# Performance work log

Hardware: AMD Instinct MI355X
Metric: run time of the kernel (lower is better)

The kernel has to match this reference:

```python
import jax, jax.numpy as jnp
import numpy as np

B, S, H, L, NH, F, V = 8, 512, 768, 12, 12, 3072, 21128
DH = H // NH
SEP = 102
NEG = -1e9  # eager BERT additive mask: (1-mask)*large_negative


def _ln(x, g, b, eps=1e-12):
    m = jnp.mean(x, axis=-1, keepdims=True)
    v = jnp.var(x, axis=-1, keepdims=True)
    return (x - m) * jax.lax.rsqrt(v + eps) * g + b


def _mask_bias(input_ids):
    # prefix-LM mask: tokens <= first SEP fully bidirectional; suffix causal + sees prefix
    hit = input_ids == SEP                      # [B,S]
    has_sep = jnp.any(hit, axis=1)              # [B]
    first = jnp.argmax(hit, axis=1)             # [B] (first SEP position)
    sep = jnp.minimum(first, S - 2)             # clamp as in torch code
    pos = jnp.arange(S)
    i = pos[None, :, None]
    j = pos[None, None, :]
    sb = sep[:, None, None]
    vis = (j <= sb) | ((i > sb) & (j <= i))     # [B,S,S]
    vis = jnp.where(has_sep[:, None, None], vis, True)  # no SEP -> full ones
    return jnp.where(vis, 0.0, NEG).astype(jnp.float32)[:, None]  # [B,1,S,S]


def setup_inputs():
    key = jax.random.key(0)
    ks = jax.random.split(key, 4)
    input_ids = jax.random.randint(ks[0], (B, S), 0, V)
    sep_pos = jax.random.randint(ks[1], (B,), 32, 128)
    input_ids = input_ids.at[jnp.arange(B), sep_pos].set(SEP)
    labels = jax.random.randint(ks[2], (B, S), 0, V)
    pk = jax.random.split(ks[3], 10)
    n = lambda k, sh: jax.random.normal(k, sh, jnp.float32) * 0.02
    return dict(
        input_ids=input_ids, labels=labels,
        word_emb=n(pk[0], (V, H)), pos_emb=n(pk[1], (S, H)), type_emb=n(pk[2], (2, H)),
        emb_g=jnp.ones((H,), jnp.float32), emb_b=jnp.zeros((H,), jnp.float32),
        Wq=n(pk[3], (L, H, H)), bq=jnp.zeros((L, H), jnp.float32),
        Wk=n(pk[4], (L, H, H)), bk=jnp.zeros((L, H), jnp.float32),
        Wv=n(pk[5], (L, H, H)), bv=jnp.zeros((L, H), jnp.float32),
        Wo=n(pk[6], (L, H, H)), bo=jnp.zeros((L, H), jnp.float32),
        ln1_g=jnp.ones((L, H), jnp.float32), ln1_b=jnp.zeros((L, H), jnp.float32),
        W1=n(pk[7], (L, H, F)), b1=jnp.zeros((L, F), jnp.float32),
        W2=n(pk[8], (L, F, H)), b2=jnp.zeros((L, H), jnp.float32),
        ln2_g=jnp.ones((L, H), jnp.float32), ln2_b=jnp.zeros((L, H), jnp.float32),
        cls_W=n(pk[9], (H, V)), cls_b=jnp.zeros((V,), jnp.float32),
    )


def reference(input_ids, labels, word_emb, pos_emb, type_emb, emb_g, emb_b,
              Wq, bq, Wk, bk, Wv, bv, Wo, bo, ln1_g, ln1_b,
              W1, b1, W2, b2, ln2_g, ln2_b, cls_W, cls_b):
    bias = _mask_bias(input_ids)                               # [B,1,S,S]
    x = word_emb[input_ids] + pos_emb[None, :S] + type_emb[0]  # [B,S,H]
    x = _ln(x, emb_g, emb_b)

    def layer(h, p):
        wq, bq_, wk, bk_, wv, bv_, wo, bo_, g1, g1b, w1, bb1, w2, bb2, g2, g2b = p
        heads = lambda t: t.reshape(B, S, NH, DH).transpose(0, 2, 1, 3)
        q = heads(h @ wq + bq_)
        k = heads(h @ wk + bk_)
        v = heads(h @ wv + bv_)
        scores = jnp.einsum('bhqd,bhkd->bhqk', q, k) / np.sqrt(DH).astype(np.float32) + bias
        probs = jax.nn.softmax(scores, axis=-1)
        ctx = jnp.einsum('bhqk,bhkd->bhqd', probs, v).transpose(0, 2, 1, 3).reshape(B, S, H)
        h = _ln(h + ctx @ wo + bo_, g1, g1b)
        ffn = jax.nn.gelu(h @ w1 + bb1, approximate=False) @ w2 + bb2
        h = _ln(h + ffn, g2, g2b)
        return h, None

    x, _ = jax.lax.scan(layer, x, (Wq, bq, Wk, bk, Wv, bv, Wo, bo,
                                   ln1_g, ln1_b, W1, b1, W2, b2, ln2_g, ln2_b))
    logits = x @ cls_W + cls_b                                 # [B,S,V]

    # per-sample CE: mean over tokens after first SEP; full-sequence CE if no SEP
    logp = jax.nn.log_softmax(logits, axis=-1)
    ce = -jnp.take_along_axis(logp, labels[..., None], axis=-1)[..., 0]  # [B,S]
    hit = input_ids == SEP
    has_sep = jnp.any(hit, axis=1)
    first = jnp.argmax(hit, axis=1)
    pos = jnp.arange(S)[None]
    m = jnp.where(has_sep[:, None], pos > first[:, None], True).astype(ce.dtype)
    per_sample = jnp.sum(ce * m, axis=1) / jnp.sum(m, axis=1)
    return jnp.mean(per_sample)
```

## Files before the change

### kernel.cpp

```cpp
#include <hip/hip_runtime.h>
#include <math.h>

typedef unsigned short ushort;
typedef __bf16 bf16x8 __attribute__((ext_vector_type(8)));
typedef float f32x4 __attribute__((ext_vector_type(4)));

constexpr int Bb  = 8;
constexpr int Ss  = 512;
constexpr int Hh  = 768;
constexpr int Ll  = 12;
constexpr int NHh = 12;
constexpr int Ff  = 3072;
constexpr int Vv  = 21128;
constexpr int DHh = 64;
constexpr int Mm  = Bb * Ss;
constexpr int SEP_ID = 102;
constexpr int VP  = 21504;
constexpr int NCH = 24;
constexpr int TPC = 7;
constexpr int QKVN = 3 * Hh;
constexpr float LSE_SHIFT = 20.0f;

static __device__ __forceinline__ ushort f2bf(float f) {
    unsigned u = __float_as_uint(f);
    unsigned r = (u + 0x7fffu + ((u >> 16) & 1u)) >> 16;
    return (ushort)r;
}
static __device__ __forceinline__ float bf2f(unsigned x) {
    return __uint_as_float(x << 16);
}

__global__ __launch_bounds__(512) void sep_kernel(const int* __restrict__ ids,
                                                  int* __restrict__ info)
{
    int b = blockIdx.x;
    int t = threadIdx.x;
    int v = (ids[b * Ss + t] == SEP_ID) ? t : 0x7FFFFFFF;
    #pragma unroll
    for (int off = 32; off; off >>= 1) {
        int o = __shfl_xor(v, off);
        v = min(v, o);
    }
    __shared__ int wmin[8];
    int lane = t & 63, wid = t >> 6;
    if (lane == 0) wmin[wid] = v;
    __syncthreads();
    if (t == 0) {
        int first = wmin[0];
        #pragma unroll
        for (int w = 1; w < 8; w++) first = min(first, wmin[w]);
        int has = (first != 0x7FFFFFFF) ? 1 : 0;
        info[b * 4 + 0] = first;
        info[b * 4 + 1] = has;
        info[b * 4 + 2] = has ? min(first, Ss - 2) : (Ss + 1);
    }
}

__global__ __launch_bounds__(256) void embed_ln_kernel(
    const int* __restrict__ ids, const float* __restrict__ we,
    const float* __restrict__ pe, const float* __restrict__ te,
    const float* __restrict__ g, const float* __restrict__ bp,
    float* __restrict__ x, ushort* __restrict__ xb)
{
    int tok = blockIdx.x;
    int s = tok & (Ss - 1);
    int tid = threadIdx.x;
    int id = ids[tok];
    float e[3];
    #pragma unroll
    for (int r = 0; r < 3; r++) {
        int h = tid + (r << 8);
        e[r] = we[(size_t)id * Hh + h] + pe[(size_t)s * Hh + h] + te[h];
    }
    float sum = e[0] + e[1] + e[2];
    float sq  = fmaf(e[0], e[0], fmaf(e[1], e[1], e[2] * e[2]));
    #pragma unroll
    for (int off = 32; off; off >>= 1) {
        sum += __shfl_xor(sum, off);
        sq  += __shfl_xor(sq, off);
    }
    __shared__ float red[8];
    int lane = tid & 63, wid = tid >> 6;
    if (lane == 0) { red[wid] = sum; red[4 + wid] = sq; }
    __syncthreads();
    sum = red[0] + red[1] + red[2] + red[3];
    sq  = red[4] + red[5] + red[6] + red[7];
    float mean = sum * (1.0f / Hh);
    float var  = sq * (1.0f / Hh) - mean * mean;
    float rstd = rsqrtf(var + 1e-12f);
    #pragma unroll
    for (int r = 0; r < 3; r++) {
        int h = tid + (r << 8);
        float v = (e[r] - mean) * rstd * g[h] + bp[h];
        x[(size_t)tok * Hh + h] = v;
        xb[(size_t)tok * Hh + h] = f2bf(v);
    }
}

__global__ __launch_bounds__(256) void resid_ln_kernel(
    const float* __restrict__ resid, const float* __restrict__ y,
    const float* __restrict__ g, const float* __restrict__ bp,
    float* __restrict__ out, ushort* __restrict__ outb)
{
    int tok = blockIdx.x;
    int tid = threadIdx.x;
    float e[3];
    #pragma unroll
    for (int r = 0; r < 3; r++) {
        int h = tid + (r << 8);
        size_t idx = (size_t)tok * Hh + h;
        e[r] = resid[idx] + y[idx];
    }
    float sum = e[0] + e[1] + e[2];
    float sq  = fmaf(e[0], e[0], fmaf(e[1], e[1], e[2] * e[2]));
    #pragma unroll
    for (int off = 32; off; off >>= 1) {
        sum += __shfl_xor(sum, off);
        sq  += __shfl_xor(sq, off);
    }
    __shared__ float red[8];
    int lane = tid & 63, wid = tid >> 6;
    if (lane == 0) { red[wid] = sum; red[4 + wid] = sq; }
    __syncthreads();
    sum = red[0] + red[1] + red[2] + red[3];
    sq  = red[4] + red[5] + red[6] + red[7];
    float mean = sum * (1.0f / Hh);
    float var  = sq * (1.0f / Hh) - mean * mean;
    float rstd = rsqrtf(var + 1e-12f);
    #pragma unroll
    for (int r = 0; r < 3; r++) {
        int h = tid + (r << 8);
        float v = (e[r] - mean) * rstd * g[h] + bp[h];
        out[(size_t)tok * Hh + h] = v;
        outb[(size_t)tok * Hh + h] = f2bf(v);
    }
}

__global__ __launch_bounds__(256) void resid_ln4_kernel(
    const float* __restrict__ resid, const float* __restrict__ p,
    const float* __restrict__ bias, const float* __restrict__ g,
    const float* __restrict__ bp,
    float* __restrict__ out, ushort* __restrict__ outb)
{
    const size_t MHl = (size_t)Mm * Hh;
    int tok = blockIdx.x;
    int tid = threadIdx.x;
    float e[3];
    #pragma unroll
    for (int r = 0; r < 3; r++) {
        int h = tid + (r << 8);
        size_t idx = (size_t)tok * Hh + h;
        float acc = resid[idx] + bias[h];
        acc += p[idx];
        acc += p[MHl + idx];
        acc += p[2 * MHl + idx];
        acc += p[3 * MHl + idx];
        e[r] = acc;
    }
    float sum = e[0] + e[1] + e[2];
    float sq  = fmaf(e[0], e[0], fmaf(e[1], e[1], e[2] * e[2]));
    #pragma unroll
    for (int off = 32; off; off >>= 1) {
        sum += __shfl_xor(sum, off);
        sq  += __shfl_xor(sq, off);
    }
    __shared__ float red[8];
    int lane = tid & 63, wid = tid >> 6;
    if (lane == 0) { red[wid] = sum; red[4 + wid] = sq; }
    __syncthreads();
    sum = red[0] + red[1] + red[2] + red[3];
    sq  = red[4] + red[5] + red[6] + red[7];
    float mean = sum * (1.0f / Hh);
    float var  = sq * (1.0f / Hh) - mean * mean;
    float rstd = rsqrtf(var + 1e-12f);
    #pragma unroll
    for (int r = 0; r < 3; r++) {
        int h = tid + (r << 8);
        float v = (e[r] - mean) * rstd * g[h] + bp[h];
        out[(size_t)tok * Hh + h] = v;
        outb[(size_t)tok * Hh + h] = f2bf(v);
    }
}

__global__ __launch_bounds__(256) void transpose_kernel(
    const float* __restrict__ W, ushort* __restrict__ Wt, int K, int N)
{
    __shared__ float ts[32][33];
    int n0 = blockIdx.x * 32, k0 = blockIdx.y * 32;
    int tx = threadIdx.x & 31, ty = threadIdx.x >> 5;
    #pragma unroll
    for (int i = 0; i < 32; i += 8)
        ts[ty + i][tx] = W[(size_t)(k0 + ty + i) * N + n0 + tx];
    __syncthreads();
    #pragma unroll
    for (int i = 0; i < 32; i += 8)
        Wt[(size_t)(n0 + ty + i) * K + k0 + tx] = f2bf(ts[tx][ty + i]);
}

__global__ __launch_bounds__(256) void transpose4_kernel(
    const float* __restrict__ s0, const float* __restrict__ s1,
    const float* __restrict__ s2, const float* __restrict__ s3,
    ushort* __restrict__ dst)
{
    const float* srcs[4] = { s0, s1, s2, s3 };
    const float* W = srcs[blockIdx.z];
    ushort* Wt = dst + (size_t)blockIdx.z * Hh * Hh;
    __shared__ float ts[32][33];
    int n0 = blockIdx.x * 32, k0 = blockIdx.y * 32;
    int tx = threadIdx.x & 31, ty = threadIdx.x >> 5;
    #pragma unroll
    for (int i = 0; i < 32; i += 8)
        ts[ty + i][tx] = W[(size_t)(k0 + ty + i) * Hh + n0 + tx];
    __syncthreads();
    #pragma unroll
    for (int i = 0; i < 32; i += 8)
        Wt[(size_t)(n0 + ty + i) * Hh + k0 + tx] = f2bf(ts[tx][ty + i]);
}

__global__ __launch_bounds__(256) void pad_transpose_kernel(
    const float* __restrict__ W, ushort* __restrict__ Wt, int K, int N)
{
    __shared__ float ts[32][33];
    int n0 = blockIdx.x * 32, k0 = blockIdx.y * 32;
    int tx = threadIdx.x & 31, ty = threadIdx.x >> 5;
    #pragma unroll
    for (int i = 0; i < 32; i += 8) {
        int n = n0 + tx;
        ts[ty + i][tx] = (n < N) ? W[(size_t)(k0 + ty + i) * N + n] : 0.f;
    }
    __syncthreads();
    #pragma unroll
    for (int i = 0; i < 32; i += 8)
        Wt[(size_t)(n0 + ty + i) * K + k0 + tx] = f2bf(ts[tx][ty + i]);
}

__global__ __launch_bounds__(256) void bias_pad_kernel(
    const float* __restrict__ cb, float* __restrict__ cbp)
{
    int i = blockIdx.x * 256 + threadIdx.x;
    if (i < VP) cbp[i] = (i < Vv) ? cb[i] : -1.0e9f;
}

__global__ __launch_bounds__(256) void bias_concat_kernel(
    const float* __restrict__ a, const float* __restrict__ b,
    const float* __restrict__ c, float* __restrict__ out)
{
    int i = blockIdx.x * 256 + threadIdx.x;
    if (i < Hh) {
        out[i] = a[i];
        out[Hh + i] = b[i];
        out[2 * Hh + i] = c[i];
    }
}

template <int ACT, int OUT_BF, int BIAS>
__global__ __launch_bounds__(256) void mfma_gemm(
    const ushort* __restrict__ A,
    const ushort* __restrict__ Bt,
    const float* __restrict__ bias,
    void* __restrict__ C,
    int N, int K, int lda, int ldb)
{
    __shared__ __align__(16) ushort As[128 * 32];
    __shared__ __align__(16) ushort Bs[128 * 32];
    const int tid = threadIdx.x;
    const int lane = tid & 63, wid = tid >> 6;
    const int m0 = blockIdx.y * 128, n0 = blockIdx.x * 128;
    const int kbase = blockIdx.z * K;
    const size_t zoff = (size_t)blockIdx.z * Mm * N;
    A += kbase;
    Bt += kbase;
    const int wr = (wid >> 1) * 64, wc = (wid & 1) * 64;
    const int lr = lane & 15;
    const int kg = (lane >> 4) << 3;

    f32x4 acc[4][4];
    #pragma unroll
    for (int mi = 0; mi < 4; ++mi)
        #pragma unroll
        for (int ni = 0; ni < 4; ++ni)
            acc[mi][ni] = (f32x4){0.f, 0.f, 0.f, 0.f};

    for (int k0 = 0; k0 < K; k0 += 32) {
        #pragma unroll
        for (int i = 0; i < 2; ++i) {
            int idx = i * 256 + tid;
            int r = idx >> 2, c = (idx & 3) << 3;
            __builtin_amdgcn_global_load_lds(
                (const __attribute__((address_space(1))) void*)(A + (size_t)(m0 + r) * lda + k0 + c),
                (__attribute__((address_space(3))) void*)(As + (size_t)(i * 256 + (wid << 6)) * 8),
                16, 0, 0);
        }
        #pragma unroll
        for (int i = 0; i < 2; ++i) {
            int idx = i * 256 + tid;
            int r = idx >> 2, c = (idx & 3) << 3;
            __builtin_amdgcn_global_load_lds(
                (const __attribute__((address_space(1))) void*)(Bt + (size_t)(n0 + r) * ldb + k0 + c),
                (__attribute__((address_space(3))) void*)(Bs + (size_t)(i * 256 + (wid << 6)) * 8),
                16, 0, 0);
        }
        __syncthreads();

        bf16x8 af[4], bfr[4];
        #pragma unroll
        for (int mi = 0; mi < 4; ++mi)
            af[mi] = *(const bf16x8*)(As + (size_t)(wr + mi * 16 + lr) * 32 + kg);
        #pragma unroll
        for (int ni = 0; ni < 4; ++ni)
            bfr[ni] = *(const bf16x8*)(Bs + (size_t)(wc + ni * 16 + lr) * 32 + kg);

        #pragma unroll
        for (int mi = 0; mi < 4; ++mi)
            #pragma unroll
            for (int ni = 0; ni < 4; ++ni)
                acc[mi][ni] = __builtin_amdgcn_mfma_f32_16x16x32_bf16(
                    af[mi], bfr[ni], acc[mi][ni], 0, 0, 0);
        __syncthreads();
    }

    #pragma unroll
    for (int ni = 0; ni < 4; ++ni) {
        int col = n0 + wc + ni * 16 + lr;
        float bsv = 0.f;
        if (BIAS) bsv = bias[col];
        #pragma unroll
        for (int mi = 0; mi < 4; ++mi) {
            f32x4 v = acc[mi][ni];
            #pragma unroll
            for (int q = 0; q < 4; ++q) {
                int row = m0 + wr + mi * 16 + ((lane >> 4) << 2) + q;
                float val = v[q] + bsv;
                if (ACT == 1) val = 0.5f * val * (1.0f + erff(val * 0.70710678118654752f));
                if (OUT_BF)
                    ((ushort*)C)[(size_t)row * N + col] = f2bf(val);
                else
                    ((float*)C)[zoff + (size_t)row * N + col] = val;
            }
        }
    }
}

constexpr int SP = 65;
constexpr int PS = 72;
constexpr int VS = 72;

__global__ __launch_bounds__(256) void flash_attn_kernel(
    const ushort* __restrict__ qkv, const int* __restrict__ info,
    ushort* __restrict__ ctx)
{
    __shared__ __align__(16) ushort K_lds[64 * 64];
    __shared__ __align__(16) ushort Vt_lds[64 * VS];
    __shared__ __align__(16) ushort P_lds[64 * PS];
    __shared__ float S_lds[64 * SP];
    __shared__ float m_s[64], l_s[64], rf_s[64];

    const int tid = threadIdx.x;
    const int lane = tid & 63, wid = tid >> 6;
    const int bh = blockIdx.y, b = bh / NHh, h = bh % NHh;
    const int i0 = blockIdx.x * 64;
    const int lr = lane & 15, hi = lane >> 4;
    const int kg = hi << 3;
    const int wr = (wid >> 1) * 32;
    const int wc = (wid & 1) * 32;
    const int has = info[b * 4 + 1], sep = info[b * 4 + 2];
    const size_t tok0 = (size_t)b * Ss;

    bf16x8 qf[2][2];
    #pragma unroll
    for (int mi = 0; mi < 2; ++mi)
        #pragma unroll
        for (int kk = 0; kk < 2; ++kk)
            qf[mi][kk] = *(const bf16x8*)&qkv[(tok0 + i0 + wr + mi * 16 + lr) * QKVN
                                             + h * DHh + kk * 32 + kg];

    f32x4 o[2][2];
    #pragma unroll
    for (int mi = 0; mi < 2; ++mi)
        #pragma unroll
        for (int ni = 0; ni < 2; ++ni)
            o[mi][ni] = (f32x4){0.f, 0.f, 0.f, 0.f};

    if (tid < 64) { m_s[tid] = -3.0e38f; l_s[tid] = 0.f; }
    __syncthreads();

    for (int j0 = 0; j0 < Ss; j0 += 64) {
        #pragma unroll
        for (int i = 0; i < 2; ++i) {
            int idx = i * 256 + tid;
            int r = idx >> 3, c = (idx & 7) << 3;
            __builtin_amdgcn_global_load_lds(
                (const __attribute__((address_space(1))) void*)
                    (qkv + (tok0 + j0 + r) * QKVN + Hh + h * DHh + c),
                (__attribute__((address_space(3))) void*)(K_lds + (size_t)idx * 8),
                16, 0, 0);
        }
        {
            int kv0 = (tid & 15) * 4;
            int d0 = (tid >> 4) * 4;
            uint2 rv[4];
            #pragma unroll
            for (int r = 0; r < 4; ++r)
                rv[r] = *(const uint2*)&qkv[(tok0 + j0 + kv0 + r) * QKVN
                                            + 2 * Hh + h * DHh + d0];
            #pragma unroll
            for (int c = 0; c < 4; ++c) {
                unsigned e0 = (c < 2) ? (rv[0].x >> (16 * c)) : (rv[0].y >> (16 * (c - 2)));
                unsigned e1 = (c < 2) ? (rv[1].x >> (16 * c)) : (rv[1].y >> (16 * (c - 2)));
                unsigned e2 = (c < 2) ? (rv[2].x >> (16 * c)) : (rv[2].y >> (16 * (c - 2)));
                unsigned e3 = (c < 2) ? (rv[3].x >> (16 * c)) : (rv[3].y >> (16 * (c - 2)));
                uint2 packed;
                packed.x = (e0 & 0xffffu) | (e1 << 16);
                packed.y = (e2 & 0xffffu) | (e3 << 16);
                *(uint2*)&Vt_lds[(size_t)(d0 + c) * VS + kv0] = packed;
            }
        }
        __syncthreads();

        f32x4 s[2][2];
        #pragma unroll
        for (int mi = 0; mi < 2; ++mi)
            #pragma unroll
            for (int ni = 0; ni < 2; ++ni)
                s[mi][ni] = (f32x4){0.f, 0.f, 0.f, 0.f};
        #pragma unroll
        for (int ni = 0; ni < 2; ++ni)
            #pragma unroll
            for (int kk = 0; kk < 2; ++kk) {
                bf16x8 kf = *(const bf16x8*)&K_lds[(size_t)(wc + ni * 16 + lr) * 64
                                                   + kk * 32 + kg];
                #pragma unroll
                for (int mi = 0; mi < 2; ++mi)
                    s[mi][ni] = __builtin_amdgcn_mfma_f32_16x16x32_bf16(
                        qf[mi][kk], kf, s[mi][ni], 0, 0, 0);
            }
        #pragma unroll
        for (int mi = 0; mi < 2; ++mi)
            #pragma unroll
            for (int ni = 0; ni < 2; ++ni)
                #pragma unroll
                for (int q = 0; q < 4; ++q) {
                    int rl = wr + mi * 16 + hi * 4 + q;
                    int cl = wc + ni * 16 + lr;
                    int gi = i0 + rl, gj = j0 + cl;
                    bool vis = (!has) || (gj <= sep) || ((gi > sep) && (gj <= gi));
                    S_lds[rl * SP + cl] = s[mi][ni][q] * 0.125f
                                          + (vis ? 0.0f : -1000000000.0f);
                }
        __syncthreads();

        {
            int r = tid >> 2, c0 = (tid & 3) * 16;
            float mold = m_s[r];
            float sv[16];
            float tmax = -3.0e38f;
            #pragma unroll
            for (int c = 0; c < 16; ++c) {
                sv[c] = S_lds[r * SP + c0 + c];
                tmax = fmaxf(tmax, sv[c]);
            }
            tmax = fmaxf(tmax, __shfl_xor(tmax, 1));
            tmax = fmaxf(tmax, __shfl_xor(tmax, 2));
            float mnew = fmaxf(mold, tmax);
            float sum = 0.f;
            #pragma unroll
            for (int c = 0; c < 16; ++c) {
                float p = __expf(sv[c] - mnew);
                P_lds[r * PS + c0 + c] = f2bf(p);
                sum += p;
            }
            sum += __shfl_xor(sum, 1);
            sum += __shfl_xor(sum, 2);
            if ((tid & 3) == 0) {
                float rf = __expf(mold - mnew);
                rf_s[r] = rf;
                l_s[r] = l_s[r] * rf + sum;
                m_s[r] = mnew;
            }
        }
        __syncthreads();

        #pragma unroll
        for (int mi = 0; mi < 2; ++mi)
            #pragma unroll
            for (int q = 0; q < 4; ++q) {
                float rf = rf_s[wr + mi * 16 + hi * 4 + q];
                #pragma unroll
                for (int ni = 0; ni < 2; ++ni)
                    o[mi][ni][q] *= rf;
            }
        #pragma unroll
        for (int kk = 0; kk < 2; ++kk) {
            bf16x8 pf[2];
            #pragma unroll
            for (int mi = 0; mi < 2; ++mi)
                pf[mi] = *(const bf16x8*)&P_lds[(size_t)(wr + mi * 16 + lr) * PS
                                                + kk * 32 + kg];
            #pragma unroll
            for (int ni = 0; ni < 2; ++ni) {
                bf16x8 vf = *(const bf16x8*)&Vt_lds[(size_t)(wc + ni * 16 + lr) * VS
                                                    + kk * 32 + kg];
                #pragma unroll
                for (int mi = 0; mi < 2; ++mi)
                    o[mi][ni] = __builtin_amdgcn_mfma_f32_16x16x32_bf16(
                        pf[mi], vf, o[mi][ni], 0, 0, 0);
            }
        }
        __syncthreads();
    }

    #pragma unroll
    for (int mi = 0; mi < 2; ++mi)
        #pragma unroll
        for (int q = 0; q < 4; ++q) {
            int rl = wr + mi * 16 + hi * 4 + q;
            float inv = 1.0f / l_s[rl];
            #pragma unroll
            for (int ni = 0; ni < 2; ++ni)
                ctx[(tok0 + i0 + rl) * Hh + h * DHh + wc + ni * 16 + lr]
                    = f2bf(o[mi][ni][q] * inv);
        }
}

__global__ __launch_bounds__(256) void cls_lse_kernel(
    const ushort* __restrict__ A,
    const ushort* __restrict__ WT,
    const float* __restrict__ cbp,
    const int* __restrict__ labels,
    float* __restrict__ psv, float* __restrict__ pll)
{
    __shared__ __align__(16) ushort As[128 * 32];
    __shared__ __align__(16) ushort Bs[128 * 32];
    __shared__ float ssum[2][128];
    __shared__ float sll[128];
    __shared__ int lab[128];
    const int tid = threadIdx.x;
    const int lane = tid & 63, wid = tid >> 6;
    const int m0 = blockIdx.y * 128;
    const int chunk = blockIdx.x;
    if (tid < 128) {
        sll[tid] = 0.f;
        lab[tid] = labels[m0 + tid];
    }
    const int wr = (wid >> 1) * 64, wcid = wid & 1, wc = wcid * 64;
    const int lr = lane & 15;
    const int hi = lane >> 4;
    const int kg = hi << 3;

    float sacc[16];
    #pragma unroll
    for (int i = 0; i < 16; ++i) sacc[i] = 0.f;

    for (int t = 0; t < TPC; ++t) {
        const int n0 = (chunk * TPC + t) * 128;
        f32x4 acc[4][4];
        #pragma unroll
        for (int mi = 0; mi < 4; ++mi)
            #pragma unroll
            for (int ni = 0; ni < 4; ++ni)
                acc[mi][ni] = (f32x4){0.f, 0.f, 0.f, 0.f};

        for (int k0 = 0; k0 < Hh; k0 += 32) {
            #pragma unroll
            for (int i = 0; i < 2; ++i) {
                int idx = i * 256 + tid;
                int r = idx >> 2, c = (idx & 3) << 3;
                __builtin_amdgcn_global_load_lds(
                    (const __attribute__((address_space(1))) void*)(A + (size_t)(m0 + r) * Hh + k0 + c),
                    (__attribute__((address_space(3))) void*)(As + (size_t)(i * 256 + (wid << 6)) * 8),
                    16, 0, 0);
            }
            #pragma unroll
            for (int i = 0; i < 2; ++i) {
                int idx = i * 256 + tid;
                int r = idx >> 2, c = (idx & 3) << 3;
                __builtin_amdgcn_global_load_lds(
                    (const __attribute__((address_space(1))) void*)(WT + (size_t)(n0 + r) * Hh + k0 + c),
                    (__attribute__((address_space(3))) void*)(Bs + (size_t)(i * 256 + (wid << 6)) * 8),
                    16, 0, 0);
            }
            __syncthreads();

            bf16x8 af[4], bfr[4];
            #pragma unroll
            for (int mi = 0; mi < 4; ++mi)
                af[mi] = *(const bf16x8*)(As + (size_t)(wr + mi * 16 + lr) * 32 + kg);
            #pragma unroll
            for (int ni = 0; ni < 4; ++ni)
                bfr[ni] = *(const bf16x8*)(Bs + (size_t)(wc + ni * 16 + lr) * 32 + kg);

            #pragma unroll
            for (int mi = 0; mi < 4; ++mi)
                #pragma unroll
                for (int ni = 0; ni < 4; ++ni)
                    acc[mi][ni] = __builtin_amdgcn_mfma_f32_16x16x32_bf16(
                        af[mi], bfr[ni], acc[mi][ni], 0, 0, 0);
            __syncthreads();
        }

        float bvs[4];
        int cols[4];
        #pragma unroll
        for (int ni = 0; ni < 4; ++ni) {
            cols[ni] = n0 + wc + ni * 16 + lr;
            bvs[ni] = cbp[cols[ni]];
        }
        #pragma unroll
        for (int mi = 0; mi < 4; ++mi) {
            #pragma unroll
            for (int q = 0; q < 4; ++q) {
                int rl = wr + mi * 16 + hi * 4 + q;
                float v0 = acc[mi][0][q] + bvs[0];
                float v1 = acc[mi][1][q] + bvs[1];
                float v2 = acc[mi][2][q] + bvs[2];
                float v3 = acc[mi][3][q] + bvs[3];
                int lb = lab[rl];
                if (lb == cols[0]) sll[rl] = v0;
                if (lb == cols[1]) sll[rl] = v1;
                if (lb == cols[2]) sll[rl] = v2;
                if (lb == cols[3]) sll[rl] = v3;
                sacc[mi * 4 + q] += __expf(v0 - LSE_SHIFT) + __expf(v1 - LSE_SHIFT)
                                  + __expf(v2 - LSE_SHIFT) + __expf(v3 - LSE_SHIFT);
            }
        }
    }

    #pragma unroll
    for (int mi = 0; mi < 4; ++mi) {
        #pragma unroll
        for (int q = 0; q < 4; ++q) {
            float s = sacc[mi * 4 + q];
            s += __shfl_xor(s, 1);
            s += __shfl_xor(s, 2);
            s += __shfl_xor(s, 4);
            s += __shfl_xor(s, 8);
            if (lr == 0) ssum[wcid][wr + mi * 16 + hi * 4 + q] = s;
        }
    }
    __syncthreads();
    if (tid < 128) {
        psv[(size_t)chunk * Mm + m0 + tid] = ssum[0][tid] + ssum[1][tid];
        pll[(size_t)chunk * Mm + m0 + tid] = sll[tid];
    }
}

__global__ __launch_bounds__(256) void cls_merge_kernel(
    const float* __restrict__ psv, const float* __restrict__ pll,
    float* __restrict__ ce)
{
    int row = blockIdx.x * 256 + threadIdx.x;
    float s = 0.f, l = 0.f;
    #pragma unroll 1
    for (int c = 0; c < NCH; ++c) {
        s += psv[(size_t)c * Mm + row];
        l += pll[(size_t)c * Mm + row];
    }
    ce[row] = (LSE_SHIFT + logf(s)) - l;
}

__global__ __launch_bounds__(256) void ce_reduce_kernel(
    const float* __restrict__ ce, const int* __restrict__ info,
    float* __restrict__ ps)
{
    int b = blockIdx.x, tid = threadIdx.x;
    int first = info[b * 4 + 0], has = info[b * 4 + 1];
    float sum = 0.0f;
    for (int s = tid; s < Ss; s += 256) {
        bool mv = has ? (s > first) : true;
        if (mv) sum += ce[b * Ss + s];
    }
    #pragma unroll
    for (int off = 32; off; off >>= 1) sum += __shfl_xor(sum, off);
    __shared__ float red[4];
    int lane = tid & 63, wid = tid >> 6;
    if (lane == 0) red[wid] = sum;
    __syncthreads();
    if (tid == 0) {
        float tot = red[0] + red[1] + red[2] + red[3];
        float cnt = has ? (float)(Ss - 1 - first) : (float)Ss;
        ps[b] = tot / cnt;
    }
}

__global__ void final_kernel(const float* __restrict__ ps, float* __restrict__ out)
{
    if (threadIdx.x == 0 && blockIdx.x == 0) {
        float t = 0.0f;
        #pragma unroll
        for (int b = 0; b < Bb; b++) t += ps[b];
        out[0] = t * (1.0f / Bb);
    }
}

extern "C" void kernel_launch(void* const* d_in, const int* in_sizes, int n_in,
                              void* d_out, int out_size, void* d_ws, size_t ws_size,
                              hipStream_t stream)
{
    const int*   ids    = (const int*)d_in[0];
    const int*   labels = (const int*)d_in[1];
    const float* we     = (const float*)d_in[2];
    const float* pe     = (const float*)d_in[3];
    const float* te     = (const float*)d_in[4];
    const float* eg     = (const float*)d_in[5];
    const float* ebp    = (const float*)d_in[6];
    const float* Wq     = (const float*)d_in[7];
    const float* bq     = (const float*)d_in[8];
    const float* Wk     = (const float*)d_in[9];
    const float* bk     = (const float*)d_in[10];
    const float* Wv     = (const float*)d_in[11];
    const float* bv     = (const float*)d_in[12];
    const float* Wo     = (const float*)d_in[13];
    const float* bo     = (const float*)d_in[14];
    const float* l1g    = (const float*)d_in[15];
    const float* l1b    = (const float*)d_in[16];
    const float* W1     = (const float*)d_in[17];
    const float* b1     = (const float*)d_in[18];
    const float* W2     = (const float*)d_in[19];
    const float* b2     = (const float*)d_in[20];
    const float* l2g    = (const float*)d_in[21];
    const float* l2b    = (const float*)d_in[22];
    const float* cW     = (const float*)d_in[23];
    const float* cbias  = (const float*)d_in[24];

    const size_t MH  = (size_t)Mm * Hh;
    const size_t MF  = (size_t)Mm * Ff;
    const size_t HHe = (size_t)Hh * Hh;
    const size_t HFe = (size_t)Hh * Ff;

    float* ws = (float*)d_ws;
    float* x      = ws;
    float* tmp    = x + MH;
    float* ce     = tmp + 4 * MH;
    float* ps     = ce + Mm;
    int*   info   = (int*)(ps + 16);
    float* bqkv   = (float*)(info + 64);
    ushort* xb    = (ushort*)(bqkv + QKVN);
    ushort* qkvb  = xb + MH;
    ushort* ctxb  = qkvb + 3 * MH;
    ushort* f1b   = ctxb + MH;
    ushort* wscr  = f1b + MF;
    ushort* wqT = wscr;
    ushort* wkT = wqT + HHe;
    ushort* wvT = wkT + HHe;
    ushort* woT = wvT + HHe;
    ushort* w1T = woT + HHe;
    ushort* w2T = w1T + HFe;
    float* clsf = (float*)(w2T + HFe);
    float* cbp  = clsf;
    float* psv  = cbp + VP;
    float* pll  = psv + (size_t)NCH * Mm;
    ushort* cWT = qkvb;

    sep_kernel<<<Bb, 512, 0, stream>>>(ids, info);
    embed_ln_kernel<<<Mm, 256, 0, stream>>>(ids, we, pe, te, eg, ebp, x, xb);

    dim3 gQKV(QKVN / 128, Mm / 128);
    dim3 gH(Hh / 128, Mm / 128);
    dim3 gF(Ff / 128, Mm / 128);
    dim3 gW2(Hh / 128, Mm / 128, 4);
    dim3 gA(Ss / 64, Bb * NHh);
    dim3 t4(Hh / 32, Hh / 32, 4);
    dim3 tHF(Ff / 32, Hh / 32);
    dim3 tFH(Hh / 32, Ff / 32);

    for (int l = 0; l < Ll; l++) {
        const float* bq_l = bq + (size_t)l * Hh;
        const float* bk_l = bk + (size_t)l * Hh;
        const float* bv_l = bv + (size_t)l * Hh;
        const float* bo_l = bo + (size_t)l * Hh;
        const float* b1_l = b1 + (size_t)l * Ff;
        const float* b2_l = b2 + (size_t)l * Hh;
        const float* g1  = l1g + (size_t)l * Hh;
        const float* be1 = l1b + (size_t)l * Hh;
        const float* g2  = l2g + (size_t)l * Hh;
        const float* be2 = l2b + (size_t)l * Hh;

        transpose4_kernel<<<t4, 256, 0, stream>>>(
            Wq + (size_t)l * HHe, Wk + (size_t)l * HHe,
            Wv + (size_t)l * HHe, Wo + (size_t)l * HHe, wscr);
        transpose_kernel<<<tHF, 256, 0, stream>>>(W1 + (size_t)l * HFe, w1T, Hh, Ff);
        transpose_kernel<<<tFH, 256, 0, stream>>>(W2 + (size_t)l * HFe, w2T, Ff, Hh);
        bias_concat_kernel<<<3, 256, 0, stream>>>(bq_l, bk_l, bv_l, bqkv);

        mfma_gemm<0, 1, 1><<<gQKV, 256, 0, stream>>>(xb, wqT, bqkv, qkvb,
                                                     QKVN, Hh, Hh, Hh);

        flash_attn_kernel<<<gA, 256, 0, stream>>>(qkvb, info, ctxb);

        mfma_gemm<0, 0, 1><<<gH, 256, 0, stream>>>(ctxb, woT, bo_l, tmp,
                                                   Hh, Hh, Hh, Hh);
        resid_ln_kernel<<<Mm, 256, 0, stream>>>(x, tmp, g1, be1, x, xb);

        mfma_gemm<1, 1, 1><<<gF, 256, 0, stream>>>(xb, w1T, b1_l, f1b,
                                                   Ff, Hh, Hh, Hh);
        mfma_gemm<0, 0, 0><<<gW2, 256, 0, stream>>>(f1b, w2T, nullptr, tmp,
                                                    Hh, Hh , Ff, Ff);
        resid_ln4_kernel<<<Mm, 256, 0, stream>>>(x, tmp, b2_l, g2, be2, x, xb);
    }

    pad_transpose_kernel<<<dim3(VP / 32, Hh / 32), 256, 0, stream>>>(cW, cWT, Hh, Vv);
    bias_pad_kernel<<<(VP + 255) / 256, 256, 0, stream>>>(cbias, cbp);
    cls_lse_kernel<<<dim3(NCH, Mm / 128), 256, 0, stream>>>(
        xb, cWT, cbp, labels, psv, pll);
    cls_merge_kernel<<<Mm / 256, 256, 0, stream>>>(psv, pll, ce);
    ce_reduce_kernel<<<Bb, 256, 0, stream>>>(ce, info, ps);
    final_kernel<<<1, 64, 0, stream>>>(ps, (float*)d_out);
}
```

Baseline: 2.721 ms.

## Merge weight prep kernels, use tanh GELU, pad K tile in LDS

Combines the per-layer weight transposes and bias concat into one prep_kernel launch to cut launch overhead. Replaces the erf GELU epilogue with a tanh-form approximation computed via exp, which is cheaper but slightly changes numerics. In attention, K is now loaded through registers into a padded LDS layout instead of direct global-to-LDS loads, aiming to reduce bank conflicts at the cost of losing async loading.

```diff
diff --git a/kernel.cpp b/kernel.cpp
--- a/kernel.cpp
+++ b/kernel.cpp
@@ -182,48 +182,61 @@
     }
 }
 
-__global__ __launch_bounds__(256) void transpose_kernel(
+__global__ __launch_bounds__(256) void prep_kernel(
+    const float* __restrict__ Wq, const float* __restrict__ Wk,
+    const float* __restrict__ Wv, const float* __restrict__ Wo,
+    const float* __restrict__ W1, const float* __restrict__ W2,
+    const float* __restrict__ bq, const float* __restrict__ bk,
+    const float* __restrict__ bv,
+    ushort* __restrict__ qkvoT, ushort* __restrict__ w1T,
+    ushort* __restrict__ w2T, float* __restrict__ bqkv)
+{
+    int b = blockIdx.x;
+    if (b >= 6912) {
+        for (int j = threadIdx.x; j < Hh; j += 256) {
+            bqkv[j]          = bq[j];
+            bqkv[Hh + j]     = bk[j];
+            bqkv[2 * Hh + j] = bv[j];
+        }
+        return;
+    }
+    const float* W;
+    ushort* Wt;
+    int K, N, n0, k0;
+    if (b < 2304) {
+        int which = b / 576, t = b % 576;
+        const float* srcs[4] = { Wq, Wk, Wv, Wo };
+        W = srcs[which];
+        Wt = qkvoT + (size_t)which * Hh * Hh;
+        K = Hh; N = Hh;
+        n0 = (t % 24) * 32; k0 = (t / 24) * 32;
+    } else if (b < 4608) {
+        int t = b - 2304;
+        W = W1; Wt = w1T; K = Hh; N = Ff;
+        n0 = (t % 96) * 32; k0 = (t / 96) * 32;
+    } else {
+        int t = b - 4608;
+        W = W2; Wt = w2T; K = Ff; N = Hh;
+        n0 = (t % 24) * 32; k0 = (t / 24) * 32;
+    }
+    __shared__ float ts[32][33];
+    int tx = threadIdx.x & 31, ty = threadIdx.x >> 5;
+    #pragma unroll
+    for (int i = 0; i < 32; i += 8)
+        ts[ty + i][tx] = W[(size_t)(k0 + ty + i) * N + n0 + tx];
+    __syncthreads();
+    #pragma unroll
+    for (int i = 0; i < 32; i += 8)
+        Wt[(size_t)(n0 + ty + i) * K + k0 + tx] = f2bf(ts[tx][ty + i]);
+}
+
+__global__ __launch_bounds__(256) void pad_transpose_kernel(
     const float* __restrict__ W, ushort* __restrict__ Wt, int K, int N)
 {
     __shared__ float ts[32][33];
     int n0 = blockIdx.x * 32, k0 = blockIdx.y * 32;
     int tx = threadIdx.x & 31, ty = threadIdx.x >> 5;
     #pragma unroll
-    for (int i = 0; i < 32; i += 8)
-        ts[ty + i][tx] = W[(size_t)(k0 + ty + i) * N + n0 + tx];
-    __syncthreads();
-    #pragma unroll
-    for (int i = 0; i < 32; i += 8)
-        Wt[(size_t)(n0 + ty + i) * K + k0 + tx] = f2bf(ts[tx][ty + i]);
-}
-
-__global__ __launch_bounds__(256) void transpose4_kernel(
-    const float* __restrict__ s0, const float* __restrict__ s1,
-    const float* __restrict__ s2, const float* __restrict__ s3,
-    ushort* __restrict__ dst)
-{
-    const float* srcs[4] = { s0, s1, s2, s3 };
-    const float* W = srcs[blockIdx.z];
-    ushort* Wt = dst + (size_t)blockIdx.z * Hh * Hh;
-    __shared__ float ts[32][33];
-    int n0 = blockIdx.x * 32, k0 = blockIdx.y * 32;
-    int tx = threadIdx.x & 31, ty = threadIdx.x >> 5;
-    #pragma unroll
-    for (int i = 0; i < 32; i += 8)
-        ts[ty + i][tx] = W[(size_t)(k0 + ty + i) * Hh + n0 + tx];
-    __syncthreads();
-    #pragma unroll
-    for (int i = 0; i < 32; i += 8)
-        Wt[(size_t)(n0 + ty + i) * Hh + k0 + tx] = f2bf(ts[tx][ty + i]);
-}
-
-__global__ __launch_bounds__(256) void pad_transpose_kernel(
-    const float* __restrict__ W, ushort* __restrict__ Wt, int K, int N)
-{
-    __shared__ float ts[32][33];
-    int n0 = blockIdx.x * 32, k0 = blockIdx.y * 32;
-    int tx = threadIdx.x & 31, ty = threadIdx.x >> 5;
-    #pragma unroll
     for (int i = 0; i < 32; i += 8) {
         int n = n0 + tx;
         ts[ty + i][tx] = (n < N) ? W[(size_t)(k0 + ty + i) * N + n] : 0.f;
@@ -239,18 +252,6 @@
 {
     int i = blockIdx.x * 256 + threadIdx.x;
     if (i < VP) cbp[i] = (i < Vv) ? cb[i] : -1.0e9f;
-}
-
-__global__ __launch_bounds__(256) void bias_concat_kernel(
-    const float* __restrict__ a, const float* __restrict__ b,
-    const float* __restrict__ c, float* __restrict__ out)
-{
-    int i = blockIdx.x * 256 + threadIdx.x;
-    if (i < Hh) {
-        out[i] = a[i];
-        out[Hh + i] = b[i];
-        out[2 * Hh + i] = c[i];
-    }
 }
 
 template <int ACT, int OUT_BF, int BIAS>
@@ -331,7 +332,11 @@
             for (int q = 0; q < 4; ++q) {
                 int row = m0 + wr + mi * 16 + ((lane >> 4) << 2) + q;
                 float val = v[q] + bsv;
-                if (ACT == 1) val = 0.5f * val * (1.0f + erff(val * 0.70710678118654752f));
+                if (ACT == 1) {
+                    float y = 0.7978845608028654f
+                              * (val + 0.044715f * val * val * val);
+                    val = val / (1.0f + __expf(-2.0f * y));
+                }
                 if (OUT_BF)
                     ((ushort*)C)[(size_t)row * N + col] = f2bf(val);
                 else
@@ -349,7 +354,7 @@
     const ushort* __restrict__ qkv, const int* __restrict__ info,
     ushort* __restrict__ ctx)
 {
-    __shared__ __align__(16) ushort K_lds[64 * 64];
+    __shared__ __align__(16) ushort K_lds[64 * VS];
     __shared__ __align__(16) ushort Vt_lds[64 * VS];
     __shared__ __align__(16) ushort P_lds[64 * PS];
     __shared__ float S_lds[64 * SP];
@@ -387,13 +392,10 @@
     for (int j0 = 0; j0 < Ss; j0 += 64) {
         #pragma unroll
         for (int i = 0; i < 2; ++i) {
-            int idx = i * 256 + tid;
-            int r = idx >> 3, c = (idx & 7) << 3;
-            __builtin_amdgcn_global_load_lds(
-                (const __attribute__((address_space(1))) void*)
-                    (qkv + (tok0 + j0 + r) * QKVN + Hh + h * DHh + c),
-                (__attribute__((address_space(3))) void*)(K_lds + (size_t)idx * 8),
-                16, 0, 0);
+            int ix = i * 256 + tid;
+            int r = ix >> 3, c = (ix & 7) << 3;
+            uint4 kq = *(const uint4*)&qkv[(tok0 + j0 + r) * QKVN + Hh + h * DHh + c];
+            *(uint4*)&K_lds[(size_t)r * VS + c] = kq;
         }
         {
             int kv0 = (tid & 15) * 4;
@@ -427,7 +429,7 @@
         for (int ni = 0; ni < 2; ++ni)
             #pragma unroll
             for (int kk = 0; kk < 2; ++kk) {
-                bf16x8 kf = *(const bf16x8*)&K_lds[(size_t)(wc + ni * 16 + lr) * 64
+                bf16x8 kf = *(const bf16x8*)&K_lds[(size_t)(wc + ni * 16 + lr) * VS
                                                    + kk * 32 + kg];
                 #pragma unroll
                 for (int mi = 0; mi < 2; ++mi)
@@ -740,10 +742,8 @@
     ushort* f1b   = ctxb + MH;
     ushort* wscr  = f1b + MF;
     ushort* wqT = wscr;
-    ushort* wkT = wqT + HHe;
-    ushort* wvT = wkT + HHe;
-    ushort* woT = wvT + HHe;
-    ushort* w1T = woT + HHe;
+    ushort* woT = wqT + 3 * HHe;
+    ushort* w1T = wscr + 4 * HHe;
     ushort* w2T = w1T + HFe;
     float* clsf = (float*)(w2T + HFe);
     float* cbp  = clsf;
@@ -759,14 +759,8 @@
     dim3 gF(Ff / 128, Mm / 128);
     dim3 gW2(Hh / 128, Mm / 128, 4);
     dim3 gA(Ss / 64, Bb * NHh);
-    dim3 t4(Hh / 32, Hh / 32, 4);
-    dim3 tHF(Ff / 32, Hh / 32);
-    dim3 tFH(Hh / 32, Ff / 32);
 
     for (int l = 0; l < Ll; l++) {
-        const float* bq_l = bq + (size_t)l * Hh;
-        const float* bk_l = bk + (size_t)l * Hh;
-        const float* bv_l = bv + (size_t)l * Hh;
         const float* bo_l = bo + (size_t)l * Hh;
         const float* b1_l = b1 + (size_t)l * Ff;
         const float* b2_l = b2 + (size_t)l * Hh;
@@ -775,12 +769,12 @@
         const float* g2  = l2g + (size_t)l * Hh;
         const float* be2 = l2b + (size_t)l * Hh;
 
-        transpose4_kernel<<<t4, 256, 0, stream>>>(
+        prep_kernel<<<6913, 256, 0, stream>>>(
             Wq + (size_t)l * HHe, Wk + (size_t)l * HHe,
-            Wv + (size_t)l * HHe, Wo + (size_t)l * HHe, wscr);
-        transpose_kernel<<<tHF, 256, 0, stream>>>(W1 + (size_t)l * HFe, w1T, Hh, Ff);
-        transpose_kernel<<<tFH, 256, 0, stream>>>(W2 + (size_t)l * HFe, w2T, Ff, Hh);
-        bias_concat_kernel<<<3, 256, 0, stream>>>(bq_l, bk_l, bv_l, bqkv);
+            Wv + (size_t)l * HHe, Wo + (size_t)l * HHe,
+            W1 + (size_t)l * HFe, W2 + (size_t)l * HFe,
+            bq + (size_t)l * Hh, bk + (size_t)l * Hh, bv + (size_t)l * Hh,
+            wscr, w1T, w2T, bqkv);
 
         mfma_gemm<0, 1, 1><<<gQKV, 256, 0, stream>>>(xb, wqT, bqkv, qkvb,
                                                      QKVN, Hh, Hh, Hh);
```

After: 2.620 ms. 3.7% less time.
